# Kernel tuning notes

Hardware: AMD Instinct MI355X
Metric: run time of the kernel (lower is better)

The kernel has to match this reference:

```python
import jax, jax.numpy as jnp
from jax import lax
import numpy as np

EPS = 1e-5  # BatchNorm eps (inference mode; dropouts are identity in eval)


def _proj(img, w, g, b, m, v, stride):
    """All-heads Conv2d(3x3, no bias) + BatchNorm (inference) fused across heads.
    img: [B, Cin, H, W]; w: [heads, Cout, Cin, 3, 3]; g/b/m/v: [heads, Cout].
    Returns [B, heads, Cout, N'] (channels-first token layout)."""
    heads, Cout, Cin = w.shape[0], w.shape[1], w.shape[2]
    y = lax.conv_general_dilated(
        img, w.reshape(heads * Cout, Cin, 3, 3),
        window_strides=(stride, stride), padding=[(1, 1), (1, 1)],
        dimension_numbers=('NCHW', 'OIHW', 'NCHW'))
    B = y.shape[0]
    N = y.shape[2] * y.shape[3]
    y = y.reshape(B, heads, Cout, N)
    scale = g / jnp.sqrt(v + EPS)               # [heads, Cout]
    shift = b - m * scale
    return y * scale[None, :, :, None] + shift[None, :, :, None]


def reference(x, y, w_conv, bn_gamma, bn_beta, bn_mean, bn_var, w_out1, w_out2, h, w):
    B, N, C = x.shape
    xi = x.reshape(B, h, w, C).transpose(0, 3, 1, 2)  # b (h w) c -> b c h w
    yi = y.reshape(B, h, w, C).transpose(0, 3, 1, 2)
    scale_attn = C ** -0.5

    def P(i, img, stride):
        return _proj(img, w_conv[i], bn_gamma[i], bn_beta[i], bn_mean[i], bn_var[i], stride)

    # torch: query1(x), query2(y), key1(y), key2(x), value1(y), value2(x)
    Q1 = P(0, xi, 2)  # [B,h,C,Nq]
    Q2 = P(1, yi, 2)
    K1 = P(2, yi, 2)
    K2 = P(3, xi, 2)
    V1 = P(4, yi, 1)  # [B,h,C,Nv]
    V2 = P(5, xi, 1)

    # channel-attention: scores are [B, heads, C, C], softmax over last axis
    s1 = jnp.einsum('bhcn,bhdn->bhcd', Q2, K1) * scale_attn
    s2 = jnp.einsum('bhcn,bhdn->bhcd', Q1, K2) * scale_attn
    p1 = jax.nn.softmax(s1, axis=-1)
    p2 = jax.nn.softmax(s2, axis=-1)

    # context [B,heads,C,Nv] -> mean over heads -> [B,Nv,C]
    c1 = jnp.einsum('bhcd,bhdn->bhcn', p1, V1).mean(axis=1).transpose(0, 2, 1)
    c2 = jnp.einsum('bhcd,bhdn->bhcn', p2, V2).mean(axis=1).transpose(0, 2, 1)

    o1 = c1 @ w_out1.T  # Linear(dim_in, dim_out, bias=False)
    o2 = c2 @ w_out2.T
    return o1, o2


def setup_inputs() -> dict:
    B, C, HEADS, H, W = 8, 256, 4, 64, 64
    key = jax.random.key(0)
    ks = jax.random.split(key, 9)
    conv_std = 1.0 / np.sqrt(C * 9)
    lin_std = 1.0 / np.sqrt(C)
    return {
        'x': jax.random.normal(ks[0], (B, H * W, C), jnp.float32),
        'y': jax.random.normal(ks[1], (B, H * W, C), jnp.float32),
        'w_conv': jax.random.normal(ks[2], (6, HEADS, C, C, 3, 3), jnp.float32) * conv_std,
        'bn_gamma': jax.random.uniform(ks[3], (6, HEADS, C), jnp.float32, 0.5, 1.5),
        'bn_beta': jax.random.normal(ks[4], (6, HEADS, C), jnp.float32) * 0.1,
        'bn_mean': jax.random.normal(ks[5], (6, HEADS, C), jnp.float32) * 0.1,
        'bn_var': jax.random.uniform(ks[6], (6, HEADS, C), jnp.float32, 0.5, 1.5),
        'w_out1': jax.random.normal(ks[7], (C, C), jnp.float32) * lin_std,
        'w_out2': jax.random.normal(ks[8], (C, C), jnp.float32) * lin_std,
        'h': H,
        'w': W,
    }
```

## Files before the change

kernel.cpp:

```cpp
#include <hip/hip_runtime.h>
#include <stdint.h>

typedef __bf16 bf16_t;
typedef __bf16 bf16x8 __attribute__((ext_vector_type(8)));
typedef float f32x4 __attribute__((ext_vector_type(4)));

#define EPSBN 1e-5f

#define OFF_XP   ((size_t)0)
#define SZ_IMG   ((size_t)8*4356*256*2)
#define OFF_YP   (OFF_XP + SZ_IMG)
#define OFF_WQS  (OFF_YP + SZ_IMG)
#define SZ_WQS   ((size_t)4*1024*2304*2)
#define OFF_WVT  (OFF_WQS + SZ_WQS)
#define SZ_WVT   ((size_t)2*2304*1024*2)
#define OFF_W1B  (OFF_WVT + SZ_WVT)
#define SZ_WO    ((size_t)65536*2)
#define OFF_W2B  (OFF_W1B + SZ_WO)
#define OFF_SHQ  (OFF_W2B + SZ_WO)
#define SZ_SHQ   ((size_t)4096*4)
#define OFF_SHV  (OFF_SHQ + SZ_SHQ)
#define SZ_SHV   ((size_t)2048*4)
#define OFF_QK   (OFF_SHV + SZ_SHV)
#define SZ_QK    ((size_t)4*8*1024*1024*2)
#define OFF_S    (OFF_QK + SZ_QK)
#define SZ_S     ((size_t)2*8*4*65536*4)
#define OFF_PT   (OFF_S + SZ_S)
#define SZ_PT    ((size_t)2*8*4*65536*2)
#define OFF_A1   (OFF_PT + SZ_PT)
#define SZ_A1    ((size_t)2*8*256*1024*2)
#define OFF_WEFF (OFF_A1 + SZ_A1)
#define SZ_WEFF  ((size_t)2*8*256*2304*2)
#define OFF_BIAS (OFF_WEFF + SZ_WEFF)
#define SZ_BIAS  ((size_t)2*8*256*4)
#define WS_NEED  (OFF_BIAS + SZ_BIAS)

__device__ __forceinline__ void gload16(const bf16_t* g, bf16_t* l) {
  __builtin_amdgcn_global_load_lds(
      (const __attribute__((address_space(1))) void*)g,
      (__attribute__((address_space(3))) void*)l,
      16, 0, 0);
}

__device__ __forceinline__ int lb_off0() { return ((threadIdx.x >> 6)    ) * 512; }
__device__ __forceinline__ int lb_off1() { return ((threadIdx.x >> 6) + 4) * 512; }

#define SBAR0 __builtin_amdgcn_sched_barrier(0)

template<int BSRC>
__device__ __forceinline__ void gemm_core(
    const bf16_t* __restrict__ A, int ldA,
    const bf16_t* __restrict__ B, int ldB,
    int m0, int n0, int KT, f32x4 acc[4][4])
{
  __shared__ bf16_t lA[2][4096];
  __shared__ bf16_t lB[2][4096];
  const int tid  = threadIdx.x;
  const int lane = tid & 63;
  const int wv   = tid >> 6;
  const int wr   = wv >> 1, wc = wv & 1;
  const int r4   = lane >> 2;
  const int k8   = (lane & 3) * 8;

  const bf16_t* gA0 = A + (size_t)(m0 + (wv    )*16 + r4) * ldA + k8;
  const bf16_t* gA1 = A + (size_t)(m0 + (wv + 4)*16 + r4) * ldA + k8;
  const int la0 = (wv    ) * 512;
  const int la1 = (wv + 4) * 512;
  const bf16_t* gB0 = B + (size_t)(n0 + (wv    )*16 + r4) * ldB + k8;
  const bf16_t* gB1 = B + (size_t)(n0 + (wv + 4)*16 + r4) * ldB + k8;
  (void)BSRC;

#pragma unroll
  for (int i = 0; i < 4; ++i)
#pragma unroll
    for (int j = 0; j < 4; ++j)
      acc[i][j] = f32x4{0.f, 0.f, 0.f, 0.f};

  const int lr = lane & 15;
  const int lk = (lane >> 4) * 8;
  int aidx[4], bidx[4];
#pragma unroll
  for (int f = 0; f < 4; ++f) {
    aidx[f] = (wr*64 + f*16 + lr)*32 + lk;
    bidx[f] = (wc*64 + f*16 + lr)*32 + lk;
  }

  auto stage = [&](int bufp, int kt) {
    const int kb = kt * 32;
    gload16(gA0 + kb, &lA[bufp][la0]);
    gload16(gA1 + kb, &lA[bufp][la1]);
    gload16(gB0 + kb, &lB[bufp][lb_off0()]);
    gload16(gB1 + kb, &lB[bufp][lb_off1()]);
  };

  stage(0, 0);
  __syncthreads();
  int buf = 0;
  for (int kt = 0; kt < KT; ++kt) {
    if (kt + 1 < KT) stage(buf ^ 1, kt + 1);
    bf16x8 av[4], bvv[4];
#pragma unroll
    for (int f = 0; f < 4; ++f) av[f]  = *(const bf16x8*)&lA[buf][aidx[f]];
#pragma unroll
    for (int f = 0; f < 4; ++f) bvv[f] = *(const bf16x8*)&lB[buf][bidx[f]];
#pragma unroll
    for (int i = 0; i < 4; ++i)
#pragma unroll
      for (int j = 0; j < 4; ++j)
        acc[i][j] = __builtin_amdgcn_mfma_f32_16x16x32_bf16(av[i], bvv[j], acc[i][j], 0, 0, 0);
    __syncthreads();
    buf ^= 1;
  }
}

template<int STRIDE>
__device__ __forceinline__ void conv_m201_core(
    const bf16_t* __restrict__ A, const bf16_t* __restrict__ img,
    int m0, int n0, f32x4 acc[8][4])
{
  __shared__ bf16_t lA[2][2][8192];
  __shared__ bf16_t lB[2][2][8192];
  const int tid  = threadIdx.x;
  const int lane = tid & 63;
  const int w    = tid >> 6;
  const int wm   = w >> 2;
  const int wn   = w & 3;
  const int wh   = wn >> 1;
  const int wn1  = wn & 1;

#pragma unroll
  for (int f = 0; f < 8; ++f)
#pragma unroll
    for (int c = 0; c < 4; ++c)
      acc[f][c] = f32x4{0.f, 0.f, 0.f, 0.f};

  const int srow = tid >> 3;
  const int swz  = ((tid & 7) ^ (srow & 7)) * 8;
  const bf16_t* gAsrc = A + (size_t)(m0 + srow) * 2304 + swz;
  const bf16_t* gBsrc[4];
#pragma unroll
  for (int h = 0; h < 2; ++h)
#pragma unroll
    for (int c = 0; c < 2; ++c) {
      const int tok = n0 + h*128 + c*64 + srow;
      int px;
      if (STRIDE == 1) px = (tok >> 6)*66 + (tok & 63);
      else             px = ((tok >> 5)*2)*66 + (tok & 31)*2;
      gBsrc[h*2 + c] = img + (size_t)px*256 + swz;
    }

  auto stageA = [&](int T1, int h) {
    bf16_t* dst = &lA[T1 & 1][h][0] + tid*8;
    const bf16_t* src = gAsrc + (size_t)(h*128)*2304 + T1*64;
    gload16(src, dst);
    gload16(src + (size_t)64*2304, dst + 4096);
  };
  auto stageB = [&](int T1, int h) {
    const int tap = T1 >> 2;
    const int ky  = (tap >= 6) ? 2 : ((tap >= 3) ? 1 : 0);
    const int kx  = tap - ky*3;
    const int ps  = (ky*66 + kx)*256 + (T1 & 3)*64;
    bf16_t* dst = &lB[T1 & 1][h][0] + tid*8;
    gload16(gBsrc[h*2 + 0] + ps, dst);
    gload16(gBsrc[h*2 + 1] + ps, dst + 4096);
  };

  const int rb  = (lane & 15) * 64;
  const int l7  = lane & 7;
  const int g4  = lane >> 4;
  int rs[2];
  rs[0] = ((    g4) ^ l7) * 8;
  rs[1] = ((4 + g4) ^ l7) * 8;

  stageA(0, 0); stageB(0, 0); stageA(0, 1); stageB(0, 1);
  SBAR0;
  asm volatile("s_waitcnt vmcnt(0)" ::: "memory");
  SBAR0;
  __builtin_amdgcn_s_barrier();

  for (int T = 0; T < 36; ++T) {
    const int buf = T & 1;
    const bf16_t* pa = &lA[buf][wm][0];
    const bf16_t* pb = &lB[buf][wh][0];
    bf16x8 av[4][2], bvs[2][2][2];
    const bool nt = (T + 1 < 36);

#pragma unroll
    for (int j = 0; j < 2; ++j)
#pragma unroll
      for (int kh = 0; kh < 2; ++kh)
        bvs[0][j][kh] = *(const bf16x8*)(pb + (wn1*4096 + j*1024 + rb + rs[kh]));
#pragma unroll
    for (int i = 0; i < 4; ++i)
#pragma unroll
      for (int kh = 0; kh < 2; ++kh)
        av[i][kh] = *(const bf16x8*)(pa + (i*1024 + rb + rs[kh]));
    if (nt) { stageA(T+1, 0); stageB(T+1, 0); }
    SBAR0;
    asm volatile("s_waitcnt lgkmcnt(8)" ::: "memory");
    __builtin_amdgcn_s_barrier();
    asm volatile("s_waitcnt lgkmcnt(0)" ::: "memory");
    SBAR0;
    __builtin_amdgcn_s_setprio(1);
#pragma unroll
    for (int i = 0; i < 4; ++i)
#pragma unroll
      for (int j = 0; j < 2; ++j)
#pragma unroll
        for (int kh = 0; kh < 2; ++kh)
          acc[i][j] = __builtin_amdgcn_mfma_f32_16x16x32_bf16(av[i][kh], bvs[0][j][kh], acc[i][j], 0, 0, 0);
    __builtin_amdgcn_s_setprio(0);
    __builtin_amdgcn_s_barrier();

#pragma unroll
    for (int j = 0; j < 2; ++j)
#pragma unroll
      for (int kh = 0; kh < 2; ++kh)
        bvs[1][j][kh] = *(const bf16x8*)(pb + (wn1*4096 + (2+j)*1024 + rb + rs[kh]));
    if (nt) { stageA(T+1, 1); stageB(T+1, 1); }
    SBAR0;
    __builtin_amdgcn_s_barrier();
    asm volatile("s_waitcnt lgkmcnt(0)" ::: "memory");
    SBAR0;
    __builtin_amdgcn_s_setprio(1);
#pragma unroll
    for (int i = 0; i < 4; ++i)
#pragma unroll
      for (int j = 0; j < 2; ++j)
#pragma unroll
        for (int kh = 0; kh < 2; ++kh)
          acc[i][2+j] = __builtin_amdgcn_mfma_f32_16x16x32_bf16(av[i][kh], bvs[1][j][kh], acc[i][2+j], 0, 0, 0);
    __builtin_amdgcn_s_setprio(0);
    __builtin_amdgcn_s_barrier();

#pragma unroll
    for (int i = 0; i < 4; ++i)
#pragma unroll
      for (int kh = 0; kh < 2; ++kh)
        av[i][kh] = *(const bf16x8*)(pa + ((4+i)*1024 + rb + rs[kh]));
    SBAR0;
    asm volatile("s_waitcnt lgkmcnt(4)" ::: "memory");
    __builtin_amdgcn_s_barrier();
    asm volatile("s_waitcnt lgkmcnt(0)" ::: "memory");
    SBAR0;
    __builtin_amdgcn_s_setprio(1);
#pragma unroll
    for (int i = 0; i < 4; ++i)
#pragma unroll
      for (int j = 0; j < 2; ++j)
#pragma unroll
        for (int kh = 0; kh < 2; ++kh)
          acc[4+i][j] = __builtin_amdgcn_mfma_f32_16x16x32_bf16(av[i][kh], bvs[0][j][kh], acc[4+i][j], 0, 0, 0);
    __builtin_amdgcn_s_setprio(0);
    __builtin_amdgcn_s_barrier();

    SBAR0;
    asm volatile("s_waitcnt vmcnt(0)" ::: "memory");
    SBAR0;
    __builtin_amdgcn_s_barrier();
    __builtin_amdgcn_s_setprio(1);
#pragma unroll
    for (int i = 0; i < 4; ++i)
#pragma unroll
      for (int j = 0; j < 2; ++j)
#pragma unroll
        for (int kh = 0; kh < 2; ++kh)
          acc[4+i][2+j] = __builtin_amdgcn_mfma_f32_16x16x32_bf16(av[i][kh], bvs[1][j][kh], acc[4+i][2+j], 0, 0, 0);
    __builtin_amdgcn_s_setprio(0);
    __builtin_amdgcn_s_barrier();
  }
}

__global__ __launch_bounds__(512, 1) void k_conv_qk7(const bf16_t* __restrict__ wqs,
    const bf16_t* __restrict__ xp, const bf16_t* __restrict__ yp,
    bf16_t* __restrict__ qk, const float* __restrict__ shq)
{
  const int n  = blockIdx.x;
  const int b  = n & 7;
  const int r1 = n >> 3;
  const int ci = r1 & 3;
  const int r2 = r1 >> 2;
  const int nt = r2 & 3;
  const int mt = r2 >> 2;
  const int m0 = mt*256, n0 = nt*256;
  const bf16_t* A = wqs + (size_t)ci * 1024 * 2304;
  const bf16_t* img = (((ci == 0) | (ci == 3)) ? xp : yp) + (size_t)b*4356*256;
  f32x4 acc[8][4];
  conv_m201_core<2>(A, img, m0, n0, acc);

  bf16_t* out = qk + (size_t)(ci*8 + b) * 1024 * 1024;
  const float* sh = shq + ci*1024;
  const int lane = threadIdx.x & 63, w = threadIdx.x >> 6;
  const int wm = w >> 2, wn = w & 3;
#pragma unroll
  for (int f = 0; f < 8; ++f) {
    const int row0 = m0 + wm*128 + f*16 + ((lane >> 4) << 2);
    const f32x4 s4 = *(const f32x4*)&sh[row0];
#pragma unroll
    for (int c = 0; c < 4; ++c) {
      const int col = n0 + wn*64 + c*16 + (lane & 15);
#pragma unroll
      for (int r = 0; r < 4; ++r)
        out[(size_t)(row0 + r)*1024 + col] = (bf16_t)(acc[f][c][r] + s4[r]);
    }
  }
}

__global__ __launch_bounds__(512, 1) void k_conv_out7(const bf16_t* __restrict__ weff,
    const bf16_t* __restrict__ xp, const bf16_t* __restrict__ yp,
    const float* __restrict__ bias, float* __restrict__ dout)
{
  const int n  = blockIdx.x;
  const int b  = n & 7;
  const int r1 = n >> 3;
  const int br = r1 & 1;
  const int nt = r1 >> 1;
  const int n0 = nt*256;
  const bf16_t* A = weff + (size_t)(br*8 + b)*589824;
  const bf16_t* img = ((br == 0) ? yp : xp) + (size_t)b*4356*256;
  f32x4 acc[8][4];
  conv_m201_core<1>(A, img, 0, n0, acc);

  float* outp = dout + (size_t)br*8388608 + (size_t)b*1048576;
  const float* bp = bias + (size_t)(br*8 + b)*256;
  const int lane = threadIdx.x & 63, w = threadIdx.x >> 6;
  const int wm = w >> 2, wn = w & 3;
#pragma unroll
  for (int f = 0; f < 8; ++f) {
    const int e0 = wm*128 + f*16 + ((lane >> 4) << 2);
    const f32x4 bv4 = *(const f32x4*)&bp[e0];
#pragma unroll
    for (int c = 0; c < 4; ++c) {
      const int tok = n0 + wn*64 + c*16 + (lane & 15);
      f32x4 v = acc[f][c] + bv4;
      *(f32x4*)&outp[(size_t)tok*256 + e0] = v;
    }
  }
}

__global__ __launch_bounds__(256) void k_pack(const float* __restrict__ x, const float* __restrict__ y,
                                              bf16_t* __restrict__ xp, bf16_t* __restrict__ yp)
{
  const int t   = threadIdx.x;
  const int pix = blockIdx.x*4 + (t >> 6);
  const int c4  = (t & 63) * 4;
  const int b   = blockIdx.y;
  const int im  = blockIdx.z;
  const int i = pix / 66, j = pix - i*66;
  const float* src = im ? y : x;
  bf16_t* dst = im ? yp : xp;
  float4 v = make_float4(0.f, 0.f, 0.f, 0.f);
  if (i >= 1 && i <= 64 && j >= 1 && j <= 64)
    v = *(const float4*)&src[((size_t)b*4096 + (size_t)(i-1)*64 + (j-1))*256 + c4];
  bf16_t o4[4] = {(bf16_t)v.x, (bf16_t)v.y, (bf16_t)v.z, (bf16_t)v.w};
  *(uint64_t*)&dst[((size_t)b*4356 + pix)*256 + c4] = *(const uint64_t*)o4;
}

__global__ __launch_bounds__(256) void k_prep_wq(const float* __restrict__ wcv,
    const float* __restrict__ g, const float* __restrict__ be,
    const float* __restrict__ mu, const float* __restrict__ va,
    bf16_t* __restrict__ wqs, float* __restrict__ shq)
{
  const int blk = blockIdx.x;
  __shared__ float lw[2304];
  const float* src = wcv + (size_t)blk * 2304;
  for (int t = threadIdx.x; t < 2304; t += 256) lw[t] = src[t];
  const float sc = g[blk] * rsqrtf(va[blk] + EPSBN);
  if (threadIdx.x == 0) shq[blk] = be[blk] - mu[blk]*sc;
  __syncthreads();
  bf16_t* dst = wqs + (size_t)blk * 2304;
  for (int t = threadIdx.x; t < 2304; t += 256) {
    const int tap = t >> 8, c = t & 255;
    dst[t] = (bf16_t)(lw[c*9 + tap] * sc);
  }
}

__global__ __launch_bounds__(256) void k_prep_wv(const float* __restrict__ wcv,
    const float* __restrict__ g, const float* __restrict__ va,
    bf16_t* __restrict__ wvT)
{
  const int cch = blockIdx.x;
  const int h = blockIdx.y >> 2, dc = blockIdx.y & 3;
  const int br = blockIdx.z;
  __shared__ float lw[64][72];
  __shared__ float lsc[64];
  const int ci = 4 + br;
  const int c0 = cch*8, d0 = dc*64;
  for (int e = threadIdx.x; e < 64*72; e += 256) {
    const int dd = e / 72, q = e - dd*72;
    lw[dd][q] = wcv[(size_t)(ci*1024 + h*256 + d0 + dd)*2304 + c0*9 + q];
  }
  if (threadIdx.x < 64) {
    const int bnIdx = ci*1024 + h*256 + d0 + threadIdx.x;
    lsc[threadIdx.x] = g[bnIdx] * rsqrtf(va[bnIdx] + EPSBN);
  }
  __syncthreads();
  for (int e = threadIdx.x; e < 72*64; e += 256) {
    const int kq = e >> 6, dd = e & 63;
    const int cc = kq / 9, tap = kq - cc*9;
    const int kp = tap*256 + c0 + cc;
    wvT[(size_t)br*2359296 + (size_t)kp*1024 + h*256 + d0 + dd] =
        (bf16_t)(lw[dd][cc*9 + tap] * lsc[dd]);
  }
}

__global__ __launch_bounds__(256) void k_small(const float* __restrict__ w1, const float* __restrict__ w2,
    const float* __restrict__ g, const float* __restrict__ be,
    const float* __restrict__ mu, const float* __restrict__ va,
    bf16_t* __restrict__ w1b, bf16_t* __restrict__ w2b, float* __restrict__ shv)
{
  const int idx = blockIdx.x*256 + threadIdx.x;
  if (idx < 65536) {
    w1b[idx] = (bf16_t)w1[idx];
  } else if (idx < 131072) {
    w2b[idx - 65536] = (bf16_t)w2[idx - 65536];
  } else if (idx < 133120) {
    const int t = idx - 131072;
    const int bnIdx = 4096 + t;
    const float sc = g[bnIdx] * rsqrtf(va[bnIdx] + EPSBN);
    shv[t] = be[bnIdx] - mu[bnIdx]*sc;
  }
}

__global__ __launch_bounds__(256) void k_gemm_s(const bf16_t* __restrict__ qk, float* __restrict__ sb)
{
  const int bx = blockIdx.x, by = blockIdx.y, br = blockIdx.z;
  const int mt = bx >> 1, nt = bx & 1;
  const int b = by >> 2, h = by & 3;
  const int ai = (br == 0) ? 1 : 0;
  const int bi = (br == 0) ? 2 : 3;
  const bf16_t* A  = qk + ((size_t)(ai*8 + b)*1024 + h*256) * 1024;
  const bf16_t* Bp = qk + ((size_t)(bi*8 + b)*1024 + h*256) * 1024;
  f32x4 acc[4][4];
  gemm_core<0>(A, 1024, Bp, 1024, mt*128, nt*128, 32, acc);

  float* out = sb + ((size_t)(br*8 + b)*4 + h) * 65536;
  const int lane = threadIdx.x & 63, wv = threadIdx.x >> 6;
  const int wr = wv >> 1, wc = wv & 1;
#pragma unroll
  for (int i = 0; i < 4; ++i) {
    const int row0 = mt*128 + wr*64 + i*16 + ((lane >> 4) << 2);
#pragma unroll
    for (int j = 0; j < 4; ++j) {
      const int col = nt*128 + wc*64 + j*16 + (lane & 15);
#pragma unroll
      for (int r = 0; r < 4; ++r)
        out[(size_t)(row0 + r)*256 + col] = acc[i][j][r];
    }
  }
}

__global__ __launch_bounds__(256) void k_softmax(const float* __restrict__ sb, bf16_t* __restrict__ pt)
{
  const int cc = blockIdx.x;
  const int bh = blockIdx.y;
  const int br = blockIdx.z;
  const size_t base = ((size_t)br*32 + bh) * 65536;
  __shared__ bf16_t lp[32][256];
  const int tid = threadIdx.x, lane = tid & 63, wv = tid >> 6;
  for (int r = 0; r < 8; ++r) {
    const int row = wv*8 + r;
    const float* srow = sb + base + (size_t)(cc*32 + row)*256;
    f32x4 v = ((const f32x4*)srow)[lane];
    v *= 0.0625f;
    float m = fmaxf(fmaxf(v[0], v[1]), fmaxf(v[2], v[3]));
#pragma unroll
    for (int o = 32; o; o >>= 1) m = fmaxf(m, __shfl_xor(m, o));
    const float e0 = __expf(v[0]-m), e1 = __expf(v[1]-m), e2 = __expf(v[2]-m), e3 = __expf(v[3]-m);
    float s = e0+e1+e2+e3;
#pragma unroll
    for (int o = 32; o; o >>= 1) s += __shfl_xor(s, o);
    const float inv = 0.25f / s;
    lp[row][lane*4+0] = (bf16_t)(e0*inv);
    lp[row][lane*4+1] = (bf16_t)(e1*inv);
    lp[row][lane*4+2] = (bf16_t)(e2*inv);
    lp[row][lane*4+3] = (bf16_t)(e3*inv);
  }
  __syncthreads();
  bf16_t* dst = pt + base;
  for (int it = 0; it < 32; ++it) {
    const int idx = it*256 + tid;
    const int d = idx >> 5, c = idx & 31;
    dst[(size_t)d*256 + cc*32 + c] = lp[c][d];
  }
}

__global__ __launch_bounds__(256) void k_gemm_a(const bf16_t* __restrict__ w1b, const bf16_t* __restrict__ w2b,
    const bf16_t* __restrict__ pt, bf16_t* __restrict__ a1)
{
  const int bx = blockIdx.x, by = blockIdx.y, br = blockIdx.z;
  const int mt = bx >> 1, nt = bx & 1;
  const int b = by >> 2, h = by & 3;
  const bf16_t* A  = br ? w2b : w1b;
  const bf16_t* Bp = pt + ((size_t)(br*8 + b)*4 + h) * 65536;
  f32x4 acc[4][4];
  gemm_core<0>(A, 256, Bp, 256, mt*128, nt*128, 8, acc);

  bf16_t* out = a1 + (size_t)(br*8 + b)*262144 + h*256;
  const int lane = threadIdx.x & 63, wv = threadIdx.x >> 6;
  const int wr = wv >> 1, wc = wv & 1;
#pragma unroll
  for (int i = 0; i < 4; ++i) {
    const int row0 = mt*128 + wr*64 + i*16 + ((lane >> 4) << 2);
#pragma unroll
    for (int j = 0; j < 4; ++j) {
      const int col = nt*128 + wc*64 + j*16 + (lane & 15);
#pragma unroll
      for (int r = 0; r < 4; ++r)
        out[(size_t)(row0 + r)*1024 + col] = (bf16_t)acc[i][j][r];
    }
  }
}

__global__ __launch_bounds__(256) void k_bias(const bf16_t* __restrict__ a1,
    const float* __restrict__ shv, float* __restrict__ bias)
{
  const int wv = threadIdx.x >> 6, lane = threadIdx.x & 63;
  const int e = blockIdx.x*4 + wv;
  const int b = blockIdx.y, br = blockIdx.z;
  const bf16_t* row = a1 + ((size_t)(br*8 + b)*256 + e)*1024;
  const float* sv = shv + br*1024;
  float acc = 0.f;
#pragma unroll
  for (int t = 0; t < 16; ++t) {
    const int idx = t*64 + lane;
    acc += (float)row[idx] * sv[idx];
  }
#pragma unroll
  for (int o = 32; o; o >>= 1) acc += __shfl_xor(acc, o);
  if (lane == 0) bias[(size_t)(br*8 + b)*256 + e] = acc;
}

__global__ __launch_bounds__(256) void k_gemm_weff(const bf16_t* __restrict__ a1,
    const bf16_t* __restrict__ wvT, bf16_t* __restrict__ weff)
{
  const int bx = blockIdx.x, b = blockIdx.y, br = blockIdx.z;
  const int mt = bx / 18, nt = bx - mt*18;
  const bf16_t* A  = a1 + (size_t)(br*8 + b)*262144;
  const bf16_t* Bp = wvT + (size_t)br*2359296;
  f32x4 acc[4][4];
  gemm_core<0>(A, 1024, Bp, 1024, mt*128, nt*128, 32, acc);

  bf16_t* out = weff + (size_t)(br*8 + b)*589824;
  const int lane = threadIdx.x & 63, wv = threadIdx.x >> 6;
  const int wr = wv >> 1, wc = wv & 1;
#pragma unroll
  for (int i = 0; i < 4; ++i) {
    const int row0 = mt*128 + wr*64 + i*16 + ((lane >> 4) << 2);
#pragma unroll
    for (int j = 0; j < 4; ++j) {
      const int col = nt*128 + wc*64 + j*16 + (lane & 15);
#pragma unroll
      for (int r = 0; r < 4; ++r)
        out[(size_t)(row0 + r)*2304 + col] = (bf16_t)acc[i][j][r];
    }
  }
}

extern "C" void kernel_launch(void* const* d_in, const int* in_sizes, int n_in,
                              void* d_out, int out_size, void* d_ws, size_t ws_size,
                              hipStream_t stream)
{
  (void)in_sizes; (void)n_in; (void)out_size;
  const float* x   = (const float*)d_in[0];
  const float* y   = (const float*)d_in[1];
  const float* wcv = (const float*)d_in[2];
  const float* bg  = (const float*)d_in[3];
  const float* bb  = (const float*)d_in[4];
  const float* bm  = (const float*)d_in[5];
  const float* bvv = (const float*)d_in[6];
  const float* w1  = (const float*)d_in[7];
  const float* w2  = (const float*)d_in[8];
  float* out = (float*)d_out;
  char* ws = (char*)d_ws;
  if (ws_size < WS_NEED) return;

  bf16_t* xp   = (bf16_t*)(ws + OFF_XP);
  bf16_t* yp   = (bf16_t*)(ws + OFF_YP);
  bf16_t* wqs  = (bf16_t*)(ws + OFF_WQS);
  bf16_t* wvT  = (bf16_t*)(ws + OFF_WVT);
  bf16_t* w1b  = (bf16_t*)(ws + OFF_W1B);
  bf16_t* w2b  = (bf16_t*)(ws + OFF_W2B);
  float*  shq  = (float*)(ws + OFF_SHQ);
  float*  shv  = (float*)(ws + OFF_SHV);
  bf16_t* qk   = (bf16_t*)(ws + OFF_QK);
  float*  sb   = (float*)(ws + OFF_S);
  bf16_t* pt   = (bf16_t*)(ws + OFF_PT);
  bf16_t* a1   = (bf16_t*)(ws + OFF_A1);
  bf16_t* weff = (bf16_t*)(ws + OFF_WEFF);
  float*  bias = (float*)(ws + OFF_BIAS);

  k_pack     <<<dim3(1089, 8, 2), 256, 0, stream>>>(x, y, xp, yp);
  k_prep_wq  <<<dim3(4096), 256, 0, stream>>>(wcv, bg, bb, bm, bvv, wqs, shq);
  k_prep_wv  <<<dim3(32, 16, 2), 256, 0, stream>>>(wcv, bg, bvv, wvT);
  k_small    <<<dim3(520), 256, 0, stream>>>(w1, w2, bg, bb, bm, bvv, w1b, w2b, shv);
  k_conv_qk7 <<<dim3(512), 512, 0, stream>>>(wqs, xp, yp, qk, shq);
  k_gemm_s   <<<dim3(4, 32, 2), 256, 0, stream>>>(qk, sb);
  k_softmax  <<<dim3(8, 32, 2), 256, 0, stream>>>(sb, pt);
  k_gemm_a   <<<dim3(4, 32, 2), 256, 0, stream>>>(w1b, w2b, pt, a1);
  k_bias     <<<dim3(64, 8, 2), 256, 0, stream>>>(a1, shv, bias);
  k_gemm_weff<<<dim3(36, 8, 2), 256, 0, stream>>>(a1, wvT, weff);
  k_conv_out7<<<dim3(256), 512, 0, stream>>>(weff, xp, yp, bias, out);
}
```

Before: 351.1 us.

## Issue all LDS fragment loads upfront and cut per-iteration barriers in conv GEMM

The K-loop of the conv GEMM mainloop now loads both halves of the A fragments (avl/avh) and both B halves from LDS at the start of each iteration. It then issues all next-tile global stages at once and runs the four MFMA quadrants, gated only by staged lgkmcnt waits. Most of the intra-iteration workgroup barriers and the priority toggles between quadrants are removed, leaving one barrier per iteration. This aims to cut synchronisation stalls and let LDS reads overlap with MFMA. In exchange it raises register pressure from holding extra A fragments. The single barrier after vmcnt(0) must still protect double-buffer reuse, because the stage writes go to the other buffer.

```diff
diff --git a/kernel.cpp b/kernel.cpp
--- a/kernel.cpp
+++ b/kernel.cpp
@@ -182,7 +182,7 @@
     const int buf = T & 1;
     const bf16_t* pa = &lA[buf][wm][0];
     const bf16_t* pb = &lB[buf][wh][0];
-    bf16x8 av[4][2], bvs[2][2][2];
+    bf16x8 avl[4][2], avh[4][2], bvs[2][2][2];
     const bool nt = (T + 1 < 36);
 
 #pragma unroll
@@ -190,83 +190,69 @@
 #pragma unroll
       for (int kh = 0; kh < 2; ++kh)
         bvs[0][j][kh] = *(const bf16x8*)(pb + (wn1*4096 + j*1024 + rb + rs[kh]));
+    SBAR0;
 #pragma unroll
     for (int i = 0; i < 4; ++i)
 #pragma unroll
       for (int kh = 0; kh < 2; ++kh)
-        av[i][kh] = *(const bf16x8*)(pa + (i*1024 + rb + rs[kh]));
-    if (nt) { stageA(T+1, 0); stageB(T+1, 0); }
-    SBAR0;
-    asm volatile("s_waitcnt lgkmcnt(8)" ::: "memory");
-    __builtin_amdgcn_s_barrier();
-    asm volatile("s_waitcnt lgkmcnt(0)" ::: "memory");
-    SBAR0;
-    __builtin_amdgcn_s_setprio(1);
-#pragma unroll
-    for (int i = 0; i < 4; ++i)
-#pragma unroll
-      for (int j = 0; j < 2; ++j)
-#pragma unroll
-        for (int kh = 0; kh < 2; ++kh)
-          acc[i][j] = __builtin_amdgcn_mfma_f32_16x16x32_bf16(av[i][kh], bvs[0][j][kh], acc[i][j], 0, 0, 0);
-    __builtin_amdgcn_s_setprio(0);
-    __builtin_amdgcn_s_barrier();
-
+        avl[i][kh] = *(const bf16x8*)(pa + (i*1024 + rb + rs[kh]));
+    SBAR0;
 #pragma unroll
     for (int j = 0; j < 2; ++j)
 #pragma unroll
       for (int kh = 0; kh < 2; ++kh)
         bvs[1][j][kh] = *(const bf16x8*)(pb + (wn1*4096 + (2+j)*1024 + rb + rs[kh]));
-    if (nt) { stageA(T+1, 1); stageB(T+1, 1); }
-    SBAR0;
-    __builtin_amdgcn_s_barrier();
+    SBAR0;
+#pragma unroll
+    for (int i = 0; i < 4; ++i)
+#pragma unroll
+      for (int kh = 0; kh < 2; ++kh)
+        avh[i][kh] = *(const bf16x8*)(pa + ((4+i)*1024 + rb + rs[kh]));
+    SBAR0;
+    if (nt) { stageA(T+1, 0); stageB(T+1, 0); stageA(T+1, 1); stageB(T+1, 1); }
+    SBAR0;
+
+    __builtin_amdgcn_s_setprio(1);
+    asm volatile("s_waitcnt lgkmcnt(12)" ::: "memory");
+    SBAR0;
+#pragma unroll
+    for (int i = 0; i < 4; ++i)
+#pragma unroll
+      for (int j = 0; j < 2; ++j)
+#pragma unroll
+        for (int kh = 0; kh < 2; ++kh)
+          acc[i][j] = __builtin_amdgcn_mfma_f32_16x16x32_bf16(avl[i][kh], bvs[0][j][kh], acc[i][j], 0, 0, 0);
+    SBAR0;
+    asm volatile("s_waitcnt lgkmcnt(8)" ::: "memory");
+    SBAR0;
+#pragma unroll
+    for (int i = 0; i < 4; ++i)
+#pragma unroll
+      for (int j = 0; j < 2; ++j)
+#pragma unroll
+        for (int kh = 0; kh < 2; ++kh)
+          acc[i][2+j] = __builtin_amdgcn_mfma_f32_16x16x32_bf16(avl[i][kh], bvs[1][j][kh], acc[i][2+j], 0, 0, 0);
+    SBAR0;
     asm volatile("s_waitcnt lgkmcnt(0)" ::: "memory");
     SBAR0;
-    __builtin_amdgcn_s_setprio(1);
 #pragma unroll
     for (int i = 0; i < 4; ++i)
 #pragma unroll
       for (int j = 0; j < 2; ++j)
 #pragma unroll
         for (int kh = 0; kh < 2; ++kh)
-          acc[i][2+j] = __builtin_amdgcn_mfma_f32_16x16x32_bf16(av[i][kh], bvs[1][j][kh], acc[i][2+j], 0, 0, 0);
+          acc[4+i][j] = __builtin_amdgcn_mfma_f32_16x16x32_bf16(avh[i][kh], bvs[0][j][kh], acc[4+i][j], 0, 0, 0);
+#pragma unroll
+    for (int i = 0; i < 4; ++i)
+#pragma unroll
+      for (int j = 0; j < 2; ++j)
+#pragma unroll
+        for (int kh = 0; kh < 2; ++kh)
+          acc[4+i][2+j] = __builtin_amdgcn_mfma_f32_16x16x32_bf16(avh[i][kh], bvs[1][j][kh], acc[4+i][2+j], 0, 0, 0);
     __builtin_amdgcn_s_setprio(0);
-    __builtin_amdgcn_s_barrier();
-
-#pragma unroll
-    for (int i = 0; i < 4; ++i)
-#pragma unroll
-      for (int kh = 0; kh < 2; ++kh)
-        av[i][kh] = *(const bf16x8*)(pa + ((4+i)*1024 + rb + rs[kh]));
-    SBAR0;
-    asm volatile("s_waitcnt lgkmcnt(4)" ::: "memory");
-    __builtin_amdgcn_s_barrier();
-    asm volatile("s_waitcnt lgkmcnt(0)" ::: "memory");
-    SBAR0;
-    __builtin_amdgcn_s_setprio(1);
-#pragma unroll
-    for (int i = 0; i < 4; ++i)
-#pragma unroll
-      for (int j = 0; j < 2; ++j)
-#pragma unroll
-        for (int kh = 0; kh < 2; ++kh)
-          acc[4+i][j] = __builtin_amdgcn_mfma_f32_16x16x32_bf16(av[i][kh], bvs[0][j][kh], acc[4+i][j], 0, 0, 0);
-    __builtin_amdgcn_s_setprio(0);
-    __builtin_amdgcn_s_barrier();
-
     SBAR0;
     asm volatile("s_waitcnt vmcnt(0)" ::: "memory");
     SBAR0;
-    __builtin_amdgcn_s_barrier();
-    __builtin_amdgcn_s_setprio(1);
-#pragma unroll
-    for (int i = 0; i < 4; ++i)
-#pragma unroll
-      for (int j = 0; j < 2; ++j)
-#pragma unroll
-        for (int kh = 0; kh < 2; ++kh)
-          acc[4+i][2+j] = __builtin_amdgcn_mfma_f32_16x16x32_bf16(av[i][kh], bvs[1][j][kh], acc[4+i][2+j], 0, 0, 0);
-    __builtin_amdgcn_s_setprio(0);
     __builtin_amdgcn_s_barrier();
   }
 }
```

Result: faster. 327.7 us (-6.7%).
